# Kernel optimization log

Measured on AMD Instinct MI355X. Metric: run time of the kernel, lower is better.

The kernel has to match this reference:

```python
import jax, jax.numpy as jnp
import numpy as np

N = 50000        # num_nodes
E = 800000       # num_edges (before self-loops)
F_IN = 64        # node_feature_dim
HID = 128        # hidden_dim per head (layer 1)
HEADS = 4
OUT = 256        # output_dim (layer 2, heads=1)
NEG_SLOPE = 0.2  # PyG GATConv default leaky_relu slope


def setup_inputs() -> dict:
    key = jax.random.key(0)
    ks = jax.random.split(key, 10)
    edge_index = jax.random.randint(ks[0], (2, E), 0, N, dtype=jnp.int32)
    node_emb = jax.random.normal(ks[1], (N, F_IN), jnp.float32)
    # Layer 1: GATConv(64 -> 128, heads=4, concat=True)
    W1 = jax.random.normal(ks[2], (F_IN, HEADS * HID), jnp.float32) / np.sqrt(F_IN)
    a_src1 = jax.random.normal(ks[3], (HEADS, HID), jnp.float32) / np.sqrt(HID)
    a_dst1 = jax.random.normal(ks[4], (HEADS, HID), jnp.float32) / np.sqrt(HID)
    b1 = jnp.zeros((HEADS * HID,), jnp.float32)
    # Layer 2: GATConv(512 -> 256, heads=1)
    W2 = jax.random.normal(ks[5], (HEADS * HID, OUT), jnp.float32) / np.sqrt(HEADS * HID)
    a_src2 = jax.random.normal(ks[6], (1, OUT), jnp.float32) / np.sqrt(OUT)
    a_dst2 = jax.random.normal(ks[7], (1, OUT), jnp.float32) / np.sqrt(OUT)
    b2 = jnp.zeros((OUT,), jnp.float32)
    return {
        "edge_index": edge_index, "node_emb": node_emb,
        "W1": W1, "a_src1": a_src1, "a_dst1": a_dst1, "b1": b1,
        "W2": W2, "a_src2": a_src2, "a_dst2": a_dst2, "b2": b2,
        "batch_size": 1,
    }


def gat_layer(x, src, dst, W, a_src, a_dst, b, heads, ch):
    """PyG-style GATConv (concat=True, self-loops already in src/dst)."""
    n = x.shape[0]
    xw = (x @ W).reshape(n, heads, ch)                       # [N, H, C]
    alpha_s = jnp.einsum('nhc,hc->nh', xw, a_src)            # [N, H]
    alpha_d = jnp.einsum('nhc,hc->nh', xw, a_dst)            # [N, H]
    logits = jax.nn.leaky_relu(alpha_s[src] + alpha_d[dst], NEG_SLOPE)  # [Etot, H]
    # numerically stable segment softmax over edges grouped by dst
    m = jax.ops.segment_max(logits, dst, num_segments=n)     # [N, H]
    e = jnp.exp(logits - m[dst])                             # [Etot, H]
    denom = jax.ops.segment_sum(e, dst, num_segments=n)      # [N, H]
    alpha = e / denom[dst]                                   # [Etot, H]
    msg = xw[src] * alpha[:, :, None]                        # [Etot, H, C]
    out = jax.ops.segment_sum(msg, dst, num_segments=n)      # [N, H, C]
    return out.reshape(n, heads * ch) + b


def reference(edge_index, node_emb, W1, a_src1, a_dst1, b1,
              W2, a_src2, a_dst2, b2, batch_size):
    # PyG GATConv adds self-loops by default
    loop = jnp.arange(N, dtype=edge_index.dtype)
    src = jnp.concatenate([edge_index[0], loop])
    dst = jnp.concatenate([edge_index[1], loop])
    x = gat_layer(node_emb, src, dst, W1, a_src1, a_dst1, b1, HEADS, HID)
    x = jax.nn.elu(x)                                        # dropout = identity (eval)
    x = gat_layer(x, src, dst, W2, a_src2, a_dst2, b2, 1, OUT)
    g = jnp.mean(x, axis=0, keepdims=True)                   # [1, OUT]
    if batch_size > 1:
        g = jnp.broadcast_to(g, (batch_size, OUT))
    return g
```

## Files before the change

### kernel.cpp

```cpp
#include <hip/hip_runtime.h>
#include <cstdint>
#include <cstddef>

#define NEG_SLOPE 0.2f

typedef __bf16 bf16x8 __attribute__((ext_vector_type(8)));
typedef __bf16 bf16x4 __attribute__((ext_vector_type(4)));
typedef float f32x4 __attribute__((ext_vector_type(4)));

__device__ __forceinline__ int dstKeyOf(const int* ei, int E, int i) {
  return (i < E) ? ei[E + i] : (i - E);
}
__device__ __forceinline__ int srcKeyOf(const int* ei, int E, int i) {
  return (i < E) ? ei[i] : (i - E);
}

__global__ __launch_bounds__(256) void prep_front_kernel(
    const float* __restrict__ W1, const float* __restrict__ as1, const float* __restrict__ ad1,
    const float* __restrict__ W2, const float* __restrict__ as2, const float* __restrict__ ad2,
    const int* __restrict__ ei, int E, int NT, int nblk,
    float* __restrict__ Vs, float* __restrict__ Vd,
    float* __restrict__ vs2, float* __restrict__ vd2,
    __bf16* __restrict__ W1T, int* __restrict__ hist) {
  int bid = blockIdx.x, tid = threadIdx.x;
  if (bid == 0) {
    int k = tid >> 2, h = tid & 3;
    const float* w = W1 + k * 512 + h * 128;
    const float* a1 = as1 + h * 128;
    const float* a2 = ad1 + h * 128;
    float s = 0.f, d = 0.f;
    for (int c = 0; c < 128; ++c) { float wv = w[c]; s += wv * a1[c]; d += wv * a2[c]; }
    Vs[k * 4 + h] = s; Vd[k * 4 + h] = d;
  } else if (bid <= 2) {
    int k = (bid - 1) * 256 + tid;
    if (k < 512) {
      const float* w = W2 + k * 256;
      float s = 0.f, d = 0.f;
      for (int c = 0; c < 256; ++c) { float wv = w[c]; s += wv * as2[c]; d += wv * ad2[c]; }
      vs2[k] = s; vd2[k] = d;
    }
  } else if (bid <= 130) {
    int idx = (bid - 3) * 256 + tid;
    int n = idx >> 6, k = idx & 63;
    W1T[idx] = (__bf16)W1[(size_t)k * 512 + n];
  } else {
    __shared__ int h[256];
    h[tid] = 0;
    __syncthreads();
    int hblk = bid - 131;
    int sec = hblk >= nblk;
    int blk = hblk - sec * nblk;
    int base = blk * 1024;
#pragma unroll
    for (int j = 0; j < 4; ++j) {
      int i = base + j * 256 + tid;
      if (i < NT) {
        int key = sec ? srcKeyOf(ei, E, i) : dstKeyOf(ei, E, i);
        atomicAdd(&h[key >> 8], 1);
      }
    }
    __syncthreads();
    hist[(size_t)(sec * 256 + tid) * nblk + blk] = h[tid];
  }
}

__global__ void emb_prep_kernel(const float* __restrict__ emb, const float* __restrict__ Vs,
                                const float* __restrict__ Vd, __bf16* __restrict__ embb,
                                float* __restrict__ as_, float* __restrict__ ad_, int n) {
  __shared__ float sVs[256];
  __shared__ float sVd[256];
  for (int i = threadIdx.x; i < 256; i += blockDim.x) { sVs[i] = Vs[i]; sVd[i] = Vd[i]; }
  __syncthreads();
  int node = blockIdx.x * blockDim.x + threadIdx.x;
  if (node >= n) return;
  const float* xr = emb + (size_t)node * 64;
  __bf16* br = embb + (size_t)node * 64;
  float accs[4] = {}, accd[4] = {};
  for (int k = 0; k < 64; k += 4) {
    float4 xv = *(const float4*)(xr + k);
    bf16x4 o;
    o[0] = (__bf16)xv.x; o[1] = (__bf16)xv.y; o[2] = (__bf16)xv.z; o[3] = (__bf16)xv.w;
    *(bf16x4*)(br + k) = o;
#pragma unroll
    for (int h = 0; h < 4; ++h) {
      accs[h] += xv.x * sVs[(k + 0) * 4 + h] + xv.y * sVs[(k + 1) * 4 + h] +
                 xv.z * sVs[(k + 2) * 4 + h] + xv.w * sVs[(k + 3) * 4 + h];
      accd[h] += xv.x * sVd[(k + 0) * 4 + h] + xv.y * sVd[(k + 1) * 4 + h] +
                 xv.z * sVd[(k + 2) * 4 + h] + xv.w * sVd[(k + 3) * 4 + h];
    }
  }
#pragma unroll
  for (int h = 0; h < 4; ++h) {
    as_[(size_t)node * 4 + h] = accs[h];
    ad_[(size_t)node * 4 + h] = accd[h];
  }
}

__global__ __launch_bounds__(1024) void exscan1_kernel(int* __restrict__ a, int* __restrict__ bsum,
                                                       int M) {
  __shared__ int ws[16];
  int t = threadIdx.x, lane = t & 63, w = t >> 6;
  int i = blockIdx.x * 1024 + t;
  int v = (i < M) ? a[i] : 0;
  int x = v;
#pragma unroll
  for (int s = 1; s < 64; s <<= 1) {
    int tt = __shfl_up(x, s, 64);
    if (lane >= s) x += tt;
  }
  if (lane == 63) ws[w] = x;
  __syncthreads();
  int wo = 0;
  for (int k = 0; k < w; ++k) wo += ws[k];
  if (i < M) a[i] = wo + x - v;
  if (t == 1023) bsum[blockIdx.x] = wo + x;
}

__global__ __launch_bounds__(512) void exscan2_kernel(int* __restrict__ bsum, int nb) {
  __shared__ int buf[512];
  int t = threadIdx.x;
  int v = (t < nb) ? bsum[t] : 0;
  buf[t] = v;
  __syncthreads();
  for (int s = 1; s < 512; s <<= 1) {
    int x = (t >= s) ? buf[t - s] : 0;
    __syncthreads();
    buf[t] += x;
    __syncthreads();
  }
  if (t < nb) bsum[t] = buf[t] - v;
}

__device__ __forceinline__ int scannedAt(const int* hist, const int* bsum, size_t idx) {
  return hist[idx] + bsum[idx >> 10];
}

__global__ __launch_bounds__(256) void scatter1_kernel(const int* __restrict__ ei, int E, int NT,
                                                       int nblk, const int* __restrict__ hist,
                                                       const int* __restrict__ bsum,
                                                       int2* __restrict__ p1buf) {
  __shared__ int bins[256];
  int tid = threadIdx.x;
  int sec = (int)blockIdx.x >= nblk;
  int blk = blockIdx.x - sec * nblk;
  bins[tid] = scannedAt(hist, bsum, (size_t)(sec * 256 + tid) * nblk + blk);
  __syncthreads();
  int base = blk * 1024;
#pragma unroll
  for (int j = 0; j < 4; ++j) {
    int i = base + j * 256 + tid;
    if (i < NT) {
      int k, p;
      if (sec == 0) { k = dstKeyOf(ei, E, i); p = srcKeyOf(ei, E, i); }
      else          { k = srcKeyOf(ei, E, i); p = dstKeyOf(ei, E, i); }
      int pos = atomicAdd(&bins[k >> 8], 1);
      p1buf[pos] = make_int2(k, p);
    }
  }
}

__global__ __launch_bounds__(1024) void sortlow_kernel(const int* __restrict__ hist,
                                                       const int* __restrict__ bsum,
                                                       const int2* __restrict__ p1buf,
                                                       int nblk, int NT,
                                                       int* __restrict__ keyD, int* __restrict__ srcD,
                                                       int* __restrict__ keyS, int* __restrict__ dstS) {
  __shared__ int h[256];
  __shared__ int b2[256];
  int tid = threadIdx.x;
  int w = blockIdx.x;
  int sec = w >= 256;
  int d0 = w - sec * 256;
  int beg = scannedAt(hist, bsum, (size_t)(sec * 256 + d0) * nblk);
  int end = (w == 511) ? 2 * NT : scannedAt(hist, bsum, (size_t)(sec * 256 + d0 + 1) * nblk);
  if (tid < 256) h[tid] = 0;
  __syncthreads();
  for (int i = beg + tid; i < end; i += 1024) atomicAdd(&h[p1buf[i].x & 255], 1);
  __syncthreads();
  if (tid < 256) b2[tid] = h[tid];
  __syncthreads();
  for (int s = 1; s < 256; s <<= 1) {
    int x = (tid >= s && tid < 256) ? b2[tid - s] : 0;
    __syncthreads();
    if (tid < 256) b2[tid] += x;
    __syncthreads();
  }
  if (tid < 256) b2[tid] = beg + b2[tid] - h[tid];
  __syncthreads();
  for (int i = beg + tid; i < end; i += 1024) {
    int2 it = p1buf[i];
    int pos = atomicAdd(&b2[it.x & 255], 1);
    if (sec == 0) { keyD[pos] = it.x; srcD[pos] = it.y; }
    else          { keyS[pos - NT] = it.x; dstS[pos - NT] = it.y; }
  }
}

__global__ __launch_bounds__(256) void post_sort_kernel(
    const int* __restrict__ keyD, const int* __restrict__ srcD, const int* __restrict__ keyS,
    const float* __restrict__ as1, const float* __restrict__ ad1,
    float4* __restrict__ ew4, int* __restrict__ off, int* __restrict__ offS,
    int NT, int n, int ewBlocks) {
  if ((int)blockIdx.x < ewBlocks) {
    int i = blockIdx.x * 256 + threadIdx.x;
    if (i >= NT) return;
    int s = srcD[i], d = keyD[i];
    float4 a = *(const float4*)(as1 + (size_t)s * 4);
    float4 b = *(const float4*)(ad1 + (size_t)d * 4);
    float l0 = a.x + b.x; l0 = l0 >= 0.f ? l0 : NEG_SLOPE * l0;
    float l1 = a.y + b.y; l1 = l1 >= 0.f ? l1 : NEG_SLOPE * l1;
    float l2 = a.z + b.z; l2 = l2 >= 0.f ? l2 : NEG_SLOPE * l2;
    float l3 = a.w + b.w; l3 = l3 >= 0.f ? l3 : NEG_SLOPE * l3;
    ew4[i] = make_float4(__expf(l0), __expf(l1), __expf(l2), __expf(l3));
  } else {
    int x = (blockIdx.x - ewBlocks) * 256 + threadIdx.x;
    if (x == 0) { off[n] = NT; offS[n] = NT; }
    if (x >= 2 * n) return;
    int sec = x >= n;
    int d = x - sec * n;
    const int* key = sec ? keyS : keyD;
    int lo = 0, hi = NT;
    while (lo < hi) {
      int mid = (lo + hi) >> 1;
      if (key[mid] < d) lo = mid + 1; else hi = mid;
    }
    if (sec) offS[d] = lo; else off[d] = lo;
  }
}

__global__ __launch_bounds__(128) void agg_emb_kernel(
    const int* __restrict__ off, const int* __restrict__ srcD,
    const float4* __restrict__ ew4, const __bf16* __restrict__ embb,
    __bf16* __restrict__ aggE) {
  int d = blockIdx.x * 2 + (threadIdx.x >> 6);
  int lane = threadIdx.x & 63;
  int g = lane >> 4, p = lane & 15;
  float acc[4][4] = {};
  float wsum[4] = {};
  int beg = off[d], end = off[d + 1];
  for (int i0 = beg; i0 < end; i0 += 8) {
    int iA = i0 + g, iB = i0 + 4 + g;
    int idxA = (iA < end) ? iA : (end - 1);
    int idxB = (iB < end) ? iB : (end - 1);
    float vmA = (iA < end) ? 1.f : 0.f;
    float vmB = (iB < end) ? 1.f : 0.f;
    int sA = srcD[idxA];
    int sB = srcD[idxB];
    float4 wAv = ew4[idxA];
    float4 wBv = ew4[idxB];
    bf16x4 vA = *(const bf16x4*)(embb + (size_t)sA * 64 + p * 4);
    bf16x4 vB = *(const bf16x4*)(embb + (size_t)sB * 64 + p * 4);
    float wA0 = wAv.x * vmA, wA1 = wAv.y * vmA, wA2 = wAv.z * vmA, wA3 = wAv.w * vmA;
    float wB0 = wBv.x * vmB, wB1 = wBv.y * vmB, wB2 = wBv.z * vmB, wB3 = wBv.w * vmB;
    float fA0 = (float)vA[0], fA1 = (float)vA[1], fA2 = (float)vA[2], fA3 = (float)vA[3];
    float fB0 = (float)vB[0], fB1 = (float)vB[1], fB2 = (float)vB[2], fB3 = (float)vB[3];
    acc[0][0] += wA0 * fA0; acc[0][1] += wA0 * fA1; acc[0][2] += wA0 * fA2; acc[0][3] += wA0 * fA3;
    acc[1][0] += wA1 * fA0; acc[1][1] += wA1 * fA1; acc[1][2] += wA1 * fA2; acc[1][3] += wA1 * fA3;
    acc[2][0] += wA2 * fA0; acc[2][1] += wA2 * fA1; acc[2][2] += wA2 * fA2; acc[2][3] += wA2 * fA3;
    acc[3][0] += wA3 * fA0; acc[3][1] += wA3 * fA1; acc[3][2] += wA3 * fA2; acc[3][3] += wA3 * fA3;
    acc[0][0] += wB0 * fB0; acc[0][1] += wB0 * fB1; acc[0][2] += wB0 * fB2; acc[0][3] += wB0 * fB3;
    acc[1][0] += wB1 * fB0; acc[1][1] += wB1 * fB1; acc[1][2] += wB1 * fB2; acc[1][3] += wB1 * fB3;
    acc[2][0] += wB2 * fB0; acc[2][1] += wB2 * fB1; acc[2][2] += wB2 * fB2; acc[2][3] += wB2 * fB3;
    acc[3][0] += wB3 * fB0; acc[3][1] += wB3 * fB1; acc[3][2] += wB3 * fB2; acc[3][3] += wB3 * fB3;
    wsum[0] += wA0 + wB0; wsum[1] += wA1 + wB1; wsum[2] += wA2 + wB2; wsum[3] += wA3 + wB3;
  }
#pragma unroll
  for (int h = 0; h < 4; ++h) {
#pragma unroll
    for (int c = 0; c < 4; ++c) {
      acc[h][c] += __shfl_xor(acc[h][c], 16, 64);
      acc[h][c] += __shfl_xor(acc[h][c], 32, 64);
    }
    wsum[h] += __shfl_xor(wsum[h], 16, 64);
    wsum[h] += __shfl_xor(wsum[h], 32, 64);
  }
  if (g == 0) {
#pragma unroll
    for (int h = 0; h < 4; ++h) {
      float inv = 1.0f / wsum[h];
      bf16x4 o;
      o[0] = (__bf16)(acc[h][0] * inv); o[1] = (__bf16)(acc[h][1] * inv);
      o[2] = (__bf16)(acc[h][2] * inv); o[3] = (__bf16)(acc[h][3] * inv);
      *(bf16x4*)(aggE + (size_t)d * 256 + h * 64 + p * 4) = o;
    }
  }
}

__global__ __launch_bounds__(256) void gemm1p_kernel(const __bf16* __restrict__ aggE,
                                                     const __bf16* __restrict__ W1T,
                                                     const float* __restrict__ b1,
                                                     const float* __restrict__ vs2,
                                                     const float* __restrict__ vd2,
                                                     __bf16* __restrict__ x1,
                                                     float* __restrict__ as2p,
                                                     float* __restrict__ ad2p, int M) {
  __shared__ __bf16 Asl[128 * 72];
  __shared__ __bf16 Bsl[128 * 72];
  int tid = threadIdx.x;
  int h = blockIdx.z;
  int m0 = blockIdx.x * 128;
  int wave = tid >> 6, lane = tid & 63;
  int wm = (wave >> 1) * 64, wn = (wave & 1) * 64;
  int l15 = lane & 15, kg = lane >> 4;
#pragma unroll
  for (int i = 0; i < 4; ++i) {
    int c = tid + i * 256;
    int row = c >> 3, off = (c & 7) * 8;
    bf16x8 va = {};
    int gr = m0 + row;
    if (gr < M) va = *(const bf16x8*)(aggE + (size_t)gr * 256 + h * 64 + off);
    *(bf16x8*)(&Asl[row * 72 + off]) = va;
    bf16x8 vb = *(const bf16x8*)(W1T + ((size_t)h * 128 + row) * 64 + off);
    *(bf16x8*)(&Bsl[row * 72 + off]) = vb;
  }
  __syncthreads();
  f32x4 acc[4][4] = {};
#pragma unroll
  for (int ks = 0; ks < 2; ++ks) {
    bf16x8 af[4], bfr[4];
#pragma unroll
    for (int f = 0; f < 4; ++f) {
      af[f]  = *(const bf16x8*)(&Asl[(wm + f * 16 + l15) * 72 + kg * 8 + ks * 32]);
      bfr[f] = *(const bf16x8*)(&Bsl[(wn + f * 16 + l15) * 72 + kg * 8 + ks * 32]);
    }
#pragma unroll
    for (int i = 0; i < 4; ++i)
#pragma unroll
      for (int j = 0; j < 4; ++j)
        acc[i][j] = __builtin_amdgcn_mfma_f32_16x16x32_bf16(af[i], bfr[j], acc[i][j], 0, 0, 0);
  }
  float bv[4], vsv[4], vdv[4];
#pragma unroll
  for (int j = 0; j < 4; ++j) {
    int col = h * 128 + wn + j * 16 + l15;
    bv[j] = b1[col]; vsv[j] = vs2[col]; vdv[j] = vd2[col];
  }
  int slab = h * 2 + (wn >> 6);
#pragma unroll
  for (int i = 0; i < 4; ++i)
#pragma unroll
    for (int r = 0; r < 4; ++r) {
      int lrow = wm + i * 16 + kg * 4 + r;
      int row = m0 + lrow;
      bool vrow = row < M;
      float ps = 0.f, pd = 0.f;
#pragma unroll
      for (int j = 0; j < 4; ++j) {
        float a = acc[i][j][r] + bv[j];
        a = a > 0.f ? a : __expf(a) - 1.f;
        __bf16 xb = (__bf16)a;
        if (vrow) x1[(size_t)row * 512 + h * 128 + wn + j * 16 + l15] = xb;
        float af = (float)xb;
        ps += af * vsv[j];
        pd += af * vdv[j];
      }
      ps += __shfl_xor(ps, 1, 16); ps += __shfl_xor(ps, 2, 16);
      ps += __shfl_xor(ps, 4, 16); ps += __shfl_xor(ps, 8, 16);
      pd += __shfl_xor(pd, 1, 16); pd += __shfl_xor(pd, 2, 16);
      pd += __shfl_xor(pd, 4, 16); pd += __shfl_xor(pd, 8, 16);
      if (l15 == 0 && vrow) {
        as2p[(size_t)slab * M + row] = ps;
        ad2p[(size_t)slab * M + row] = pd;
      }
    }
}

__global__ void merge_alpha2_kernel(const float* __restrict__ as2p, const float* __restrict__ ad2p,
                                    float* __restrict__ as2, float* __restrict__ ad2, int n) {
  int i = blockIdx.x * blockDim.x + threadIdx.x;
  if (i >= n) return;
  float s = 0.f, d = 0.f;
#pragma unroll
  for (int b = 0; b < 8; ++b) {
    s += as2p[(size_t)b * n + i];
    d += ad2p[(size_t)b * n + i];
  }
  as2[i] = s; ad2[i] = d;
}

__global__ __launch_bounds__(256) void invw_kernel(
    const int* __restrict__ off, const int* __restrict__ csr_src,
    const float* __restrict__ as2, const float* __restrict__ ad2,
    float2* __restrict__ advw, float invN, int n) {
  int d = (blockIdx.x * 256 + threadIdx.x) >> 4;
  int p = threadIdx.x & 15;
  if (d >= n) return;
  float adv = ad2[d];
  int beg = off[d], end = off[d + 1];
  float wsum = 0.f;
  for (int i = beg + p; i < end; i += 16) {
    float l = as2[csr_src[i]] + adv;
    l = l >= 0.f ? l : NEG_SLOPE * l;
    wsum += __expf(l);
  }
  wsum += __shfl_xor(wsum, 1, 16); wsum += __shfl_xor(wsum, 2, 16);
  wsum += __shfl_xor(wsum, 4, 16); wsum += __shfl_xor(wsum, 8, 16);
  if (p == 0) advw[d] = make_float2(adv, invN / wsum);
}

__global__ __launch_bounds__(256) void gamma_csc_kernel(
    const int* __restrict__ offS, const int* __restrict__ csc_dst,
    const float* __restrict__ as2, const float2* __restrict__ advw,
    float* __restrict__ gamma, int n) {
  int s = (blockIdx.x * 256 + threadIdx.x) >> 4;
  int p = threadIdx.x & 15;
  if (s >= n) return;
  float as2s = as2[s];
  int beg = offS[s], end = offS[s + 1];
  float gsum = 0.f;
  for (int i = beg + p; i < end; i += 16) {
    float2 av = advw[csc_dst[i]];
    float l = as2s + av.x;
    l = l >= 0.f ? l : NEG_SLOPE * l;
    gsum += __expf(l) * av.y;
  }
  gsum += __shfl_xor(gsum, 1, 16); gsum += __shfl_xor(gsum, 2, 16);
  gsum += __shfl_xor(gsum, 4, 16); gsum += __shfl_xor(gsum, 8, 16);
  if (p == 0) gamma[s] = gsum;
}

__global__ __launch_bounds__(256) void colsum1_kernel(const __bf16* __restrict__ x1,
                                                      const float* __restrict__ gamma,
                                                      float* __restrict__ pcol, int n) {
  __shared__ float sc[512];
  int t = threadIdx.x;
  sc[t] = 0.f; sc[t + 256] = 0.f;
  __syncthreads();
  int lane = t & 63, w = t >> 6;
  float acc[8] = {};
  for (int r = blockIdx.x * 4 + w; r < n; r += gridDim.x * 4) {
    float g = gamma[r];
    bf16x8 v = *(const bf16x8*)(x1 + (size_t)r * 512 + lane * 8);
#pragma unroll
    for (int j = 0; j < 8; ++j) acc[j] += g * (float)v[j];
  }
#pragma unroll
  for (int j = 0; j < 8; ++j) atomicAdd(&sc[lane * 8 + j], acc[j]);
  __syncthreads();
  pcol[(size_t)blockIdx.x * 512 + t] = sc[t];
  pcol[(size_t)blockIdx.x * 512 + 256 + t] = sc[t + 256];
}

__global__ __launch_bounds__(256) void colsum2_kernel(const float* __restrict__ pcol,
                                                      float* __restrict__ colsum, int nb) {
  int c = threadIdx.x;
  int b0 = blockIdx.x * 16;
  float a0 = 0.f, a1 = 0.f;
#pragma unroll 4
  for (int b = b0; b < b0 + 16; ++b) {
    if (b < nb) {
      a0 += pcol[(size_t)b * 512 + c];
      a1 += pcol[(size_t)b * 512 + 256 + c];
    }
  }
  atomicAdd(&colsum[c], a0);
  atomicAdd(&colsum[c + 256], a1);
}

__global__ void final_kernel(const float* __restrict__ colsum, const float* __restrict__ W2,
                             const float* __restrict__ b2, float* __restrict__ out) {
  int c = threadIdx.x;
  int k0 = blockIdx.x * 64;
  float acc = 0.f;
  for (int k = k0; k < k0 + 64; ++k) acc += colsum[k] * W2[(size_t)k * 256 + c];
  if (blockIdx.x == 0) acc += b2[c];
  atomicAdd(&out[c], acc);
}

__global__ void bcast_kernel(float* __restrict__ dout, int total) {
  int i = blockIdx.x * blockDim.x + threadIdx.x;
  if (i >= 256 && i < total) dout[i] = dout[i & 255];
}

extern "C" void kernel_launch(void* const* d_in, const int* in_sizes, int n_in,
                              void* d_out, int out_size, void* d_ws, size_t ws_size,
                              hipStream_t stream) {
  const int* ei = (const int*)d_in[0];
  const float* emb = (const float*)d_in[1];
  const float* W1 = (const float*)d_in[2];
  const float* as1w = (const float*)d_in[3];
  const float* ad1w = (const float*)d_in[4];
  const float* b1 = (const float*)d_in[5];
  const float* W2 = (const float*)d_in[6];
  const float* as2w = (const float*)d_in[7];
  const float* ad2w = (const float*)d_in[8];
  const float* b2 = (const float*)d_in[9];
  float* out = (float*)d_out;

  const int E = in_sizes[0] / 2;
  const int N = in_sizes[1] / 64;
  const int NT = E + N;
  const int CS1 = 1024;
  const int nblk = (NT + 1023) / 1024;
  const int M = 2 * 256 * nblk;
  const int scanBlocks = (M + 1023) / 1024;

  char* ws = (char*)d_ws;
  size_t o = 0;
  auto alloc = [&](size_t bytes) { size_t r = o; o += (bytes + 255) & ~(size_t)255; return r; };
  __bf16* embb  = (__bf16*)(ws + alloc((size_t)N * 64 * 2));
  __bf16* aggE  = (__bf16*)(ws + alloc((size_t)N * 256 * 2));
  __bf16* x1    = (__bf16*)(ws + alloc((size_t)N * 512 * 2));
  __bf16* W1T   = (__bf16*)(ws + alloc((size_t)512 * 64 * 2));
  float* as1    = (float*)(ws + alloc((size_t)N * 4 * 4));
  float* ad1    = (float*)(ws + alloc((size_t)N * 4 * 4));
  float* as2    = (float*)(ws + alloc((size_t)N * 4));
  float* ad2    = (float*)(ws + alloc((size_t)N * 4));
  float* as2p   = (float*)(ws + alloc((size_t)8 * N * 4));
  float* ad2p   = (float*)(ws + alloc((size_t)8 * N * 4));
  float* pcol   = (float*)(ws + alloc((size_t)CS1 * 512 * 4));
  float2* advw  = (float2*)(ws + alloc((size_t)N * 8));
  float* gamma  = (float*)(ws + alloc((size_t)N * 4));
  int* off      = (int*)(ws + alloc((size_t)(N + 1) * 4));
  int* offS     = (int*)(ws + alloc((size_t)(N + 1) * 4));
  int* keyD     = (int*)(ws + alloc((size_t)NT * 4));
  int* srcD     = (int*)(ws + alloc((size_t)NT * 4));
  int* keyS     = (int*)(ws + alloc((size_t)NT * 4));
  int* dstS     = (int*)(ws + alloc((size_t)NT * 4));
  int2* p1buf   = (int2*)(ws + alloc((size_t)2 * NT * 8));
  int* hist     = (int*)(ws + alloc((size_t)M * 4));
  int* bsum     = (int*)(ws + alloc(512 * 4));
  float4* ew4   = (float4*)(ws + alloc((size_t)NT * 16));
  size_t zbeg = o;
  float* colsum = (float*)(ws + alloc(512 * 4));
  size_t zend = o;
  float* Vs1    = (float*)(ws + alloc(64 * 4 * 4));
  float* Vd1    = (float*)(ws + alloc(64 * 4 * 4));
  float* vs2    = (float*)(ws + alloc(512 * 4));
  float* vd2    = (float*)(ws + alloc(512 * 4));

  hipMemsetAsync(ws + zbeg, 0, zend - zbeg, stream);
  hipMemsetAsync(d_out, 0, (size_t)out_size * 4, stream);

  prep_front_kernel<<<131 + 2 * nblk, 256, 0, stream>>>(W1, as1w, ad1w, W2, as2w, ad2w,
                                                        ei, E, NT, nblk,
                                                        Vs1, Vd1, vs2, vd2, W1T, hist);
  int nb = (N + 255) / 256;
  emb_prep_kernel<<<nb, 256, 0, stream>>>(emb, Vs1, Vd1, embb, as1, ad1, N);

  exscan1_kernel<<<scanBlocks, 1024, 0, stream>>>(hist, bsum, M);
  exscan2_kernel<<<1, 512, 0, stream>>>(bsum, scanBlocks);
  scatter1_kernel<<<2 * nblk, 256, 0, stream>>>(ei, E, NT, nblk, hist, bsum, p1buf);
  sortlow_kernel<<<512, 1024, 0, stream>>>(hist, bsum, p1buf, nblk, NT, keyD, srcD, keyS, dstS);

  int ewBlocks = (NT + 255) / 256;
  int bBlocks = (2 * N + 255) / 256;
  post_sort_kernel<<<ewBlocks + bBlocks, 256, 0, stream>>>(keyD, srcD, keyS, as1, ad1,
                                                           ew4, off, offS, NT, N, ewBlocks);

  agg_emb_kernel<<<N / 2, 128, 0, stream>>>(off, srcD, ew4, embb, aggE);
  dim3 g1((N + 127) / 128, 1, 4);
  gemm1p_kernel<<<g1, 256, 0, stream>>>(aggE, W1T, b1, vs2, vd2, x1, as2p, ad2p, N);
  merge_alpha2_kernel<<<nb, 256, 0, stream>>>(as2p, ad2p, as2, ad2, N);

  invw_kernel<<<(N * 16 + 255) / 256, 256, 0, stream>>>(off, srcD, as2, ad2, advw,
                                                        1.0f / (float)N, N);
  gamma_csc_kernel<<<(N * 16 + 255) / 256, 256, 0, stream>>>(offS, dstS, as2, advw, gamma, N);
  colsum1_kernel<<<CS1, 256, 0, stream>>>(x1, gamma, pcol, N);
  colsum2_kernel<<<CS1 / 16, 256, 0, stream>>>(pcol, colsum, CS1);
  final_kernel<<<8, 256, 0, stream>>>(colsum, W2, b2, out);

  if (out_size > 256) {
    bcast_kernel<<<(out_size + 255) / 256, 256, 0, stream>>>(out, out_size);
  }
}
```

Measured before the change: 197.1 us.

## Pack edge key/value pairs into 32-bit words through sort and aggregation

Each (key, partner) edge pair is packed into one 32-bit word, 16 bits per node id, instead of an int2 or two separate int arrays. The scatter, sort, offset search, aggregation, invw and gamma kernels all read and write this packed form. This roughly halves index traffic in the sort pipeline and removes the separate key/value arrays. The agg_emb loop also moves from 8 to 16 edges per iteration via an unrolled inner loop. It relies on node ids fitting in 16 bits (N < 65536), which holds for this N but is not general.

New measurement: 204.5 us. +3.8%, slower.

```diff
diff --git a/kernel.cpp b/kernel.cpp
--- a/kernel.cpp
+++ b/kernel.cpp
@@ -138,7 +138,7 @@
 __global__ __launch_bounds__(256) void scatter1_kernel(const int* __restrict__ ei, int E, int NT,
                                                        int nblk, const int* __restrict__ hist,
                                                        const int* __restrict__ bsum,
-                                                       int2* __restrict__ p1buf) {
+                                                       unsigned* __restrict__ p1buf) {
   __shared__ int bins[256];
   int tid = threadIdx.x;
   int sec = (int)blockIdx.x >= nblk;
@@ -154,17 +154,17 @@
       if (sec == 0) { k = dstKeyOf(ei, E, i); p = srcKeyOf(ei, E, i); }
       else          { k = srcKeyOf(ei, E, i); p = dstKeyOf(ei, E, i); }
       int pos = atomicAdd(&bins[k >> 8], 1);
-      p1buf[pos] = make_int2(k, p);
+      p1buf[pos] = ((unsigned)k << 16) | (unsigned)p;
     }
   }
 }
 
 __global__ __launch_bounds__(1024) void sortlow_kernel(const int* __restrict__ hist,
                                                        const int* __restrict__ bsum,
-                                                       const int2* __restrict__ p1buf,
+                                                       const unsigned* __restrict__ p1buf,
                                                        int nblk, int NT,
-                                                       int* __restrict__ keyD, int* __restrict__ srcD,
-                                                       int* __restrict__ keyS, int* __restrict__ dstS) {
+                                                       unsigned* __restrict__ pkD,
+                                                       unsigned* __restrict__ pkS) {
   __shared__ int h[256];
   __shared__ int b2[256];
   int tid = threadIdx.x;
@@ -175,7 +175,7 @@
   int end = (w == 511) ? 2 * NT : scannedAt(hist, bsum, (size_t)(sec * 256 + d0 + 1) * nblk);
   if (tid < 256) h[tid] = 0;
   __syncthreads();
-  for (int i = beg + tid; i < end; i += 1024) atomicAdd(&h[p1buf[i].x & 255], 1);
+  for (int i = beg + tid; i < end; i += 1024) atomicAdd(&h[(p1buf[i] >> 16) & 255], 1);
   __syncthreads();
   if (tid < 256) b2[tid] = h[tid];
   __syncthreads();
@@ -188,22 +188,23 @@
   if (tid < 256) b2[tid] = beg + b2[tid] - h[tid];
   __syncthreads();
   for (int i = beg + tid; i < end; i += 1024) {
-    int2 it = p1buf[i];
-    int pos = atomicAdd(&b2[it.x & 255], 1);
-    if (sec == 0) { keyD[pos] = it.x; srcD[pos] = it.y; }
-    else          { keyS[pos - NT] = it.x; dstS[pos - NT] = it.y; }
+    unsigned pk = p1buf[i];
+    int pos = atomicAdd(&b2[(pk >> 16) & 255], 1);
+    if (sec == 0) pkD[pos] = pk;
+    else          pkS[pos - NT] = pk;
   }
 }
 
 __global__ __launch_bounds__(256) void post_sort_kernel(
-    const int* __restrict__ keyD, const int* __restrict__ srcD, const int* __restrict__ keyS,
+    const unsigned* __restrict__ pkD, const unsigned* __restrict__ pkS,
     const float* __restrict__ as1, const float* __restrict__ ad1,
     float4* __restrict__ ew4, int* __restrict__ off, int* __restrict__ offS,
     int NT, int n, int ewBlocks) {
   if ((int)blockIdx.x < ewBlocks) {
     int i = blockIdx.x * 256 + threadIdx.x;
     if (i >= NT) return;
-    int s = srcD[i], d = keyD[i];
+    unsigned pk = pkD[i];
+    int s = pk & 0xFFFF, d = pk >> 16;
     float4 a = *(const float4*)(as1 + (size_t)s * 4);
     float4 b = *(const float4*)(ad1 + (size_t)d * 4);
     float l0 = a.x + b.x; l0 = l0 >= 0.f ? l0 : NEG_SLOPE * l0;
@@ -217,18 +218,19 @@
     if (x >= 2 * n) return;
     int sec = x >= n;
     int d = x - sec * n;
-    const int* key = sec ? keyS : keyD;
+    const unsigned* key = sec ? pkS : pkD;
+    unsigned target = (unsigned)d << 16;
     int lo = 0, hi = NT;
     while (lo < hi) {
       int mid = (lo + hi) >> 1;
-      if (key[mid] < d) lo = mid + 1; else hi = mid;
+      if (key[mid] < target) lo = mid + 1; else hi = mid;
     }
     if (sec) offS[d] = lo; else off[d] = lo;
   }
 }
 
 __global__ __launch_bounds__(128) void agg_emb_kernel(
-    const int* __restrict__ off, const int* __restrict__ srcD,
+    const int* __restrict__ off, const unsigned* __restrict__ pkD,
     const float4* __restrict__ ew4, const __bf16* __restrict__ embb,
     __bf16* __restrict__ aggE) {
   int d = blockIdx.x * 2 + (threadIdx.x >> 6);
@@ -237,31 +239,24 @@
   float acc[4][4] = {};
   float wsum[4] = {};
   int beg = off[d], end = off[d + 1];
-  for (int i0 = beg; i0 < end; i0 += 8) {
-    int iA = i0 + g, iB = i0 + 4 + g;
-    int idxA = (iA < end) ? iA : (end - 1);
-    int idxB = (iB < end) ? iB : (end - 1);
-    float vmA = (iA < end) ? 1.f : 0.f;
-    float vmB = (iB < end) ? 1.f : 0.f;
-    int sA = srcD[idxA];
-    int sB = srcD[idxB];
-    float4 wAv = ew4[idxA];
-    float4 wBv = ew4[idxB];
-    bf16x4 vA = *(const bf16x4*)(embb + (size_t)sA * 64 + p * 4);
-    bf16x4 vB = *(const bf16x4*)(embb + (size_t)sB * 64 + p * 4);
-    float wA0 = wAv.x * vmA, wA1 = wAv.y * vmA, wA2 = wAv.z * vmA, wA3 = wAv.w * vmA;
-    float wB0 = wBv.x * vmB, wB1 = wBv.y * vmB, wB2 = wBv.z * vmB, wB3 = wBv.w * vmB;
-    float fA0 = (float)vA[0], fA1 = (float)vA[1], fA2 = (float)vA[2], fA3 = (float)vA[3];
-    float fB0 = (float)vB[0], fB1 = (float)vB[1], fB2 = (float)vB[2], fB3 = (float)vB[3];
-    acc[0][0] += wA0 * fA0; acc[0][1] += wA0 * fA1; acc[0][2] += wA0 * fA2; acc[0][3] += wA0 * fA3;
-    acc[1][0] += wA1 * fA0; acc[1][1] += wA1 * fA1; acc[1][2] += wA1 * fA2; acc[1][3] += wA1 * fA3;
-    acc[2][0] += wA2 * fA0; acc[2][1] += wA2 * fA1; acc[2][2] += wA2 * fA2; acc[2][3] += wA2 * fA3;
-    acc[3][0] += wA3 * fA0; acc[3][1] += wA3 * fA1; acc[3][2] += wA3 * fA2; acc[3][3] += wA3 * fA3;
-    acc[0][0] += wB0 * fB0; acc[0][1] += wB0 * fB1; acc[0][2] += wB0 * fB2; acc[0][3] += wB0 * fB3;
-    acc[1][0] += wB1 * fB0; acc[1][1] += wB1 * fB1; acc[1][2] += wB1 * fB2; acc[1][3] += wB1 * fB3;
-    acc[2][0] += wB2 * fB0; acc[2][1] += wB2 * fB1; acc[2][2] += wB2 * fB2; acc[2][3] += wB2 * fB3;
-    acc[3][0] += wB3 * fB0; acc[3][1] += wB3 * fB1; acc[3][2] += wB3 * fB2; acc[3][3] += wB3 * fB3;
-    wsum[0] += wA0 + wB0; wsum[1] += wA1 + wB1; wsum[2] += wA2 + wB2; wsum[3] += wA3 + wB3;
+  for (int i0 = beg; i0 < end; i0 += 16) {
+#pragma unroll
+    for (int q = 0; q < 4; ++q) {
+      int i = i0 + q * 4 + g;
+      int idx = (i < end) ? i : (end - 1);
+      float vm = (i < end) ? 1.f : 0.f;
+      unsigned pk = pkD[idx];
+      int s = pk & 0xFFFF;
+      float4 wv = ew4[idx];
+      bf16x4 v = *(const bf16x4*)(embb + (size_t)s * 64 + p * 4);
+      float w0 = wv.x * vm, w1 = wv.y * vm, w2 = wv.z * vm, w3 = wv.w * vm;
+      float f0 = (float)v[0], f1 = (float)v[1], f2 = (float)v[2], f3 = (float)v[3];
+      acc[0][0] += w0 * f0; acc[0][1] += w0 * f1; acc[0][2] += w0 * f2; acc[0][3] += w0 * f3;
+      acc[1][0] += w1 * f0; acc[1][1] += w1 * f1; acc[1][2] += w1 * f2; acc[1][3] += w1 * f3;
+      acc[2][0] += w2 * f0; acc[2][1] += w2 * f1; acc[2][2] += w2 * f2; acc[2][3] += w2 * f3;
+      acc[3][0] += w3 * f0; acc[3][1] += w3 * f1; acc[3][2] += w3 * f2; acc[3][3] += w3 * f3;
+      wsum[0] += w0; wsum[1] += w1; wsum[2] += w2; wsum[3] += w3;
+    }
   }
 #pragma unroll
   for (int h = 0; h < 4; ++h) {
@@ -378,7 +373,7 @@
 }
 
 __global__ __launch_bounds__(256) void invw_kernel(
-    const int* __restrict__ off, const int* __restrict__ csr_src,
+    const int* __restrict__ off, const unsigned* __restrict__ pkD,
     const float* __restrict__ as2, const float* __restrict__ ad2,
     float2* __restrict__ advw, float invN, int n) {
   int d = (blockIdx.x * 256 + threadIdx.x) >> 4;
@@ -388,7 +383,7 @@
   int beg = off[d], end = off[d + 1];
   float wsum = 0.f;
   for (int i = beg + p; i < end; i += 16) {
-    float l = as2[csr_src[i]] + adv;
+    float l = as2[pkD[i] & 0xFFFF] + adv;
     l = l >= 0.f ? l : NEG_SLOPE * l;
     wsum += __expf(l);
   }
@@ -398,7 +393,7 @@
 }
 
 __global__ __launch_bounds__(256) void gamma_csc_kernel(
-    const int* __restrict__ offS, const int* __restrict__ csc_dst,
+    const int* __restrict__ offS, const unsigned* __restrict__ pkS,
     const float* __restrict__ as2, const float2* __restrict__ advw,
     float* __restrict__ gamma, int n) {
   int s = (blockIdx.x * 256 + threadIdx.x) >> 4;
@@ -408,7 +403,7 @@
   int beg = offS[s], end = offS[s + 1];
   float gsum = 0.f;
   for (int i = beg + p; i < end; i += 16) {
-    float2 av = advw[csc_dst[i]];
+    float2 av = advw[pkS[i] & 0xFFFF];
     float l = as2s + av.x;
     l = l >= 0.f ? l : NEG_SLOPE * l;
     gsum += __expf(l) * av.y;
@@ -512,11 +507,9 @@
   float* gamma  = (float*)(ws + alloc((size_t)N * 4));
   int* off      = (int*)(ws + alloc((size_t)(N + 1) * 4));
   int* offS     = (int*)(ws + alloc((size_t)(N + 1) * 4));
-  int* keyD     = (int*)(ws + alloc((size_t)NT * 4));
-  int* srcD     = (int*)(ws + alloc((size_t)NT * 4));
-  int* keyS     = (int*)(ws + alloc((size_t)NT * 4));
-  int* dstS     = (int*)(ws + alloc((size_t)NT * 4));
-  int2* p1buf   = (int2*)(ws + alloc((size_t)2 * NT * 8));
+  unsigned* pkD = (unsigned*)(ws + alloc((size_t)NT * 4));
+  unsigned* pkS = (unsigned*)(ws + alloc((size_t)NT * 4));
+  unsigned* p1buf = (unsigned*)(ws + alloc((size_t)2 * NT * 4));
   int* hist     = (int*)(ws + alloc((size_t)M * 4));
   int* bsum     = (int*)(ws + alloc(512 * 4));
   float4* ew4   = (float4*)(ws + alloc((size_t)NT * 16));
@@ -540,21 +533,21 @@
   exscan1_kernel<<<scanBlocks, 1024, 0, stream>>>(hist, bsum, M);
   exscan2_kernel<<<1, 512, 0, stream>>>(bsum, scanBlocks);
   scatter1_kernel<<<2 * nblk, 256, 0, stream>>>(ei, E, NT, nblk, hist, bsum, p1buf);
-  sortlow_kernel<<<512, 1024, 0, stream>>>(hist, bsum, p1buf, nblk, NT, keyD, srcD, keyS, dstS);
+  sortlow_kernel<<<512, 1024, 0, stream>>>(hist, bsum, p1buf, nblk, NT, pkD, pkS);
 
   int ewBlocks = (NT + 255) / 256;
   int bBlocks = (2 * N + 255) / 256;
-  post_sort_kernel<<<ewBlocks + bBlocks, 256, 0, stream>>>(keyD, srcD, keyS, as1, ad1,
+  post_sort_kernel<<<ewBlocks + bBlocks, 256, 0, stream>>>(pkD, pkS, as1, ad1,
                                                            ew4, off, offS, NT, N, ewBlocks);
 
-  agg_emb_kernel<<<N / 2, 128, 0, stream>>>(off, srcD, ew4, embb, aggE);
+  agg_emb_kernel<<<N / 2, 128, 0, stream>>>(off, pkD, ew4, embb, aggE);
   dim3 g1((N + 127) / 128, 1, 4);
   gemm1p_kernel<<<g1, 256, 0, stream>>>(aggE, W1T, b1, vs2, vd2, x1, as2p, ad2p, N);
   merge_alpha2_kernel<<<nb, 256, 0, stream>>>(as2p, ad2p, as2, ad2, N);
 
-  invw_kernel<<<(N * 16 + 255) / 256, 256, 0, stream>>>(off, srcD, as2, ad2, advw,
+  invw_kernel<<<(N * 16 + 255) / 256, 256, 0, stream>>>(off, pkD, as2, ad2, advw,
                                                         1.0f / (float)N, N);
-  gamma_csc_kernel<<<(N * 16 + 255) / 256, 256, 0, stream>>>(offS, dstS, as2, advw, gamma, N);
+  gamma_csc_kernel<<<(N * 16 + 255) / 256, 256, 0, stream>>>(offS, pkS, as2, advw, gamma, N);
   colsum1_kernel<<<CS1, 256, 0, stream>>>(x1, gamma, pcol, N);
   colsum2_kernel<<<CS1 / 16, 256, 0, stream>>>(pcol, colsum, CS1);
   final_kernel<<<8, 256, 0, stream>>>(colsum, W2, b2, out);
```
